# Kernel tuning notes

Hardware: AMD Instinct MI355X
Metric: run time of the kernel (lower is better)

Reference implementation:

```python
import jax, jax.numpy as jnp
import numpy as np

B, N, DM, S = 128, 1024, 64, 2
D_IN = 1 + 1 + 2 + DM  # x(1) + m(1) + u(2) + h(DM)


def setup_inputs() -> dict:
    key = jax.random.key(0)
    ks = jax.random.split(key, 12)
    return {
        "x": jax.random.normal(ks[0], (B, 1, N), jnp.float32),
        "m": jax.random.uniform(ks[1], (B, 1, N), jnp.float32),
        "u": jax.random.normal(ks[2], (B, 2, N), jnp.float32),
        "h": jax.random.normal(ks[3], (B, DM, N), jnp.float32),
        # stack of support_len row-normalized-ish adjacencies [S, N, N]
        "adj": jax.random.uniform(ks[4], (S, N, N), jnp.float32) / N,
        "W_in": jax.random.normal(ks[5], (DM, D_IN), jnp.float32) * 0.05,
        "b_in": jnp.zeros((DM,), jnp.float32),
        "W_gc": jax.random.normal(ks[6], (DM, S * DM), jnp.float32) * 0.05,
        "b_gc": jnp.zeros((DM,), jnp.float32),
        "W_out": jax.random.normal(ks[7], (DM, 2 * DM), jnp.float32) * 0.05,
        "b_out": jnp.zeros((DM,), jnp.float32),
        "W_read": jax.random.normal(ks[8], (1, 2 * DM), jnp.float32) * 0.05,
        "b_read": jnp.zeros((1,), jnp.float32),
        "prelu_w": jnp.full((1,), 0.25, jnp.float32),
    }


def _conv1x1(x, W, b):
    # Conv1d(kernel_size=1): [b,c,n] x [o,c] -> [b,o,n]
    return jnp.einsum('bcn,oc->bon', x, W) + b[None, :, None]


def reference(x, m, u, h, adj, W_in, b_in, W_gc, b_gc, W_out, b_out, W_read, b_read, prelu_w):
    # concat inputs on channel dim, then 1x1 conv to d_model
    x_in = jnp.concatenate([x, m, u, h], axis=1)            # [b, d_in, n]
    x_in = _conv1x1(x_in, W_in, b_in)                        # [b, dm, n]
    # SpatialConvOrderK (order=1, include_self=False):
    # per-support aggregation einsum('ncvl,wv->ncwl') with l==1
    agg = jnp.einsum('bcv,swv->bscw', x_in, adj)             # [b, S, dm, n]
    b_, s_, c_, n_ = agg.shape
    agg = agg.reshape(b_, s_ * c_, n_)                       # support-major concat
    gc = _conv1x1(agg, W_gc, b_gc)                           # [b, dm, n]
    out = jnp.concatenate([gc, h], axis=1)                   # [b, 2dm, n]
    out = _conv1x1(out, W_out, b_out)
    out = jnp.where(out >= 0, out, prelu_w[0] * out)         # PReLU (1 param)
    out = jnp.concatenate([out, h], axis=1)                  # [b, 2dm, n]
    return _conv1x1(out, W_read, b_read), out
```

## Files before the change

kernel.cpp:

```cpp
#include <hip/hip_runtime.h>
#include <hip/hip_bf16.h>
#include <stdint.h>

#define NB 128
#define NN 1024
#define NDM 64

typedef __bf16 bf16;
typedef __bf16 bf16x8_t __attribute__((ext_vector_type(8)));
typedef __bf16 bf16x4_t __attribute__((ext_vector_type(4)));
typedef float f32x4 __attribute__((ext_vector_type(4)));

__global__ __launch_bounds__(256) void k_prep(
    const float* __restrict__ adj,
    const float* __restrict__ W_in, const float* __restrict__ b_in,
    const float* __restrict__ W_gc, const float* __restrict__ b_gc,
    const float* __restrict__ W_out, const float* __restrict__ b_out,
    const float* __restrict__ W_read,
    bf16* __restrict__ adjb, bf16* __restrict__ WAT, float* __restrict__ WYX,
    float* __restrict__ BIAS, bf16* __restrict__ W1B, bf16* __restrict__ A2B,
    float* __restrict__ HBv) {
  const int bx = blockIdx.x;
  if (bx < 2048) {
    int i = bx * 256 + threadIdx.x;
    float4 v = reinterpret_cast<const float4*>(adj)[i];
    bf16x4_t r;
    r.x = (bf16)v.x; r.y = (bf16)v.y; r.z = (bf16)v.z; r.w = (bf16)v.w;
    reinterpret_cast<bf16x4_t*>(adjb)[i] = r;
    return;
  }
  int i = (bx - 2048) * 256 + threadIdx.x;
  if (i < 8192) {
    int r = i >> 6, cc = i & 63;
    int cq = cc >> 3, j = cc & 7;
    int c = ((cq ^ (r & 7)) << 3) + j;
    int s = r >> 6, o = r & 63;
    float val = 0.f;
    for (int k = 0; k < 64; ++k) val += W_gc[o * 128 + s * 64 + k] * W_in[k * 68 + 4 + c];
    WAT[i] = (bf16)val;
  } else if (i < 8704) {
    int idx = i - 8192;
    int r = idx >> 2, jj = idx & 3;
    int s = r >> 6, o = r & 63;
    float val = 0.f;
    for (int k = 0; k < 64; ++k) val += W_gc[o * 128 + s * 64 + k] * W_in[k * 68 + jj];
    WYX[idx] = val;
  } else if (i < 8832) {
    int r = i - 8704;
    int s = r >> 6, o = r & 63;
    float val = 0.f;
    for (int k = 0; k < 64; ++k) val += W_gc[o * 128 + s * 64 + k] * b_in[k];
    BIAS[r] = val;
  } else if (i < 12928) {
    int j = i - 8832;
    int o = j >> 6, c = j & 63;
    W1B[j] = (bf16)W_out[o * 128 + c];
  } else if (i < 18048) {
    int j = i - 12928;
    int r = j >> 6, c = j & 63;
    float val = 0.f;
    if (r < 64) val = W_out[r * 128 + 64 + c];
    else if (r == 64) val = W_read[64 + c];
    A2B[j] = (bf16)val;
  } else if (i < 18112) {
    int o = i - 18048;
    float val = b_out[o];
    for (int c = 0; c < 64; ++c) val += W_out[o * 128 + c] * b_gc[c];
    HBv[o] = val;
  }
}

__global__ __launch_bounds__(256) void k_build(
    const float* __restrict__ x, const float* __restrict__ m, const float* __restrict__ u,
    const float* __restrict__ h, const bf16* __restrict__ WAT,
    const float* __restrict__ WYX, const float* __restrict__ BIAS,
    bf16* __restrict__ Y, bf16* __restrict__ HT, float* __restrict__ out2) {
  __shared__ __align__(16) float T[64 * 128];
  __shared__ __align__(16) bf16 HTs[128 * 64];
  __shared__ __align__(16) bf16 WAs[128 * 64];
  __shared__ __align__(16) float X4L[128 * 4];
  __shared__ __align__(16) float WYXs[128 * 4];
  __shared__ __align__(16) float biasL[128];
  const int t = threadIdx.x;
  const int vb = blockIdx.x * 128;
  const int b = blockIdx.y;

  for (int i = t; i < 2048; i += 256)
    __builtin_amdgcn_global_load_lds(
        (const uint32_t*)(h + (size_t)(b * 64 + (i >> 5)) * NN + vb + (i & 31) * 4),
        (uint32_t*)&T[i * 4], 16, 0, 0);
  for (int i = t; i < 1024; i += 256)
    __builtin_amdgcn_global_load_lds((const uint32_t*)(WAT + i * 8), (uint32_t*)&WAs[i * 8], 16, 0, 0);
  if (t < 128)
    __builtin_amdgcn_global_load_lds((const uint32_t*)(WYX + t * 4), (uint32_t*)&WYXs[t * 4], 16, 0, 0);
  if (t < 32)
    __builtin_amdgcn_global_load_lds((const uint32_t*)(BIAS + t * 4), (uint32_t*)&biasL[t * 4], 16, 0, 0);
  if (t < 128) {
    float4 x4;
    x4.x = x[(size_t)b * NN + vb + t];
    x4.y = m[(size_t)b * NN + vb + t];
    x4.z = u[(size_t)(b * 2) * NN + vb + t];
    x4.w = u[(size_t)(b * 2 + 1) * NN + vb + t];
    *reinterpret_cast<float4*>(&X4L[t * 4]) = x4;
  }
  __syncthreads();

  {
    const int v = t >> 1, half = t & 1;
#pragma unroll
    for (int cc = 0; cc < 4; ++cc) {
      int cq = half * 4 + cc;
      int cbase = (cq ^ (v & 7)) << 3;
      bf16x8_t pk;
#pragma unroll
      for (int j = 0; j < 8; ++j) pk[j] = (bf16)T[(cbase + j) * 128 + v];
      *reinterpret_cast<bf16x8_t*>(&HTs[v * 64 + cq * 8]) = pk;
      *reinterpret_cast<bf16x8_t*>(&HT[((size_t)(b << 10) + vb + v) * 64 + cq * 8]) = pk;
    }
  }
  for (int i = t; i < 2048; i += 256) {
    int r = i >> 5, ck = i & 31;
    float4 hv = *reinterpret_cast<const float4*>(&T[r * 128 + ck * 4]);
    *reinterpret_cast<float4*>(&out2[(size_t)(b * 128 + 64 + r) * NN + vb + ck * 4]) = hv;
  }
  __syncthreads();

  const int wave = t >> 6, lane = t & 63;
  const int q = lane >> 4, lx = lane & 7, o16 = lane & 15;
  const int offK0 = (q ^ lx) << 3, offK1 = ((q + 4) ^ lx) << 3;

#pragma unroll
  for (int vi = 0; vi < 2; ++vi) {
    const int vt = wave + vi * 4;
    const int vrow = vt * 16 + o16;
    bf16x8_t af0 = *reinterpret_cast<const bf16x8_t*>(&HTs[vrow * 64 + offK0]);
    bf16x8_t af1 = *reinterpret_cast<const bf16x8_t*>(&HTs[vrow * 64 + offK1]);
    float4 x4r[4];
#pragma unroll
    for (int r = 0; r < 4; ++r)
      x4r[r] = *reinterpret_cast<const float4*>(&X4L[(vt * 16 + q * 4 + r) * 4]);
    const int vg = vb + vt * 16 + q * 4;
    for (int nt = 0; nt < 8; ++nt) {
      const int rr = nt * 16 + o16;
      bf16x8_t bf0 = *reinterpret_cast<const bf16x8_t*>(&WAs[rr * 64 + offK0]);
      bf16x8_t bf1 = *reinterpret_cast<const bf16x8_t*>(&WAs[rr * 64 + offK1]);
      float bsv = biasL[rr];
      float4 wy = *reinterpret_cast<const float4*>(&WYXs[rr * 4]);
      f32x4 c0;
#pragma unroll
      for (int r = 0; r < 4; ++r)
        c0[r] = bsv + wy.x * x4r[r].x + wy.y * x4r[r].y + wy.z * x4r[r].z + wy.w * x4r[r].w;
      f32x4 acc = __builtin_amdgcn_mfma_f32_16x16x32_bf16(af0, bf0, c0, 0, 0, 0);
      acc = __builtin_amdgcn_mfma_f32_16x16x32_bf16(af1, bf1, acc, 0, 0, 0);
      const int s = nt >> 2;
      const int o = rr - s * 64;
      bf16x4_t pk;
      pk.x = (bf16)acc[0]; pk.y = (bf16)acc[1]; pk.z = (bf16)acc[2]; pk.w = (bf16)acc[3];
      *reinterpret_cast<bf16x4_t*>(&Y[(size_t)(b * 64 + o) * 2048 + s * 1024 + vg]) = pk;
    }
  }
}

__global__ __launch_bounds__(512, 2) void k_gemm(
    const bf16* __restrict__ Y, const bf16* __restrict__ ADJB,
    const bf16* __restrict__ HT,
    const bf16* __restrict__ W1B, const bf16* __restrict__ A2B,
    const float* __restrict__ HBv, const float* __restrict__ W_read,
    const float* __restrict__ b_read, const float* __restrict__ prelu_w,
    float* __restrict__ out0, float* __restrict__ out2) {
  __shared__ __align__(16) union SMem {
    struct { bf16 As[3][256 * 64]; bf16 Bs[3][128 * 64]; } st;
    struct {
      bf16 gcs[4 * 128 * 72];
      bf16 W1s[64 * 72];
      bf16 A2s[80 * 72];
      float HBs[64];
      float Wrs[64];
    } ep;
  } sm;

  const int t = threadIdx.x;
  const int wave = t >> 6, lane = t & 63;
  const int lin = blockIdx.y * 32 + blockIdx.x;
  const int xcd = lin & 7, rest = lin >> 3;
  const int rowA = (xcd * 4 + (rest >> 3)) * 256;
  const int colB = (rest & 7) * 128;
  const int wm = (wave >> 1) * 64, wn = (wave & 1) * 64;
  const int fr = lane & 15;
  const int q = lane >> 4, lx = lane & 7;
  const int offK0 = (q ^ lx) << 3, offK1 = ((q + 4) ^ lx) << 3;

  f32x4 acc[4][4];
  const f32x4 zero = {0.f, 0.f, 0.f, 0.f};
#pragma unroll
  for (int i = 0; i < 4; ++i)
#pragma unroll
    for (int j = 0; j < 4; ++j) acc[i][j] = zero;

  const bf16* aSrc[4]; const bf16* bSrc[2];
#pragma unroll
  for (int j = 0; j < 4; ++j) {
    const int c = t + 512 * j;
    const int row = c >> 3;
    const int qs = ((c & 7) ^ (row & 7)) << 3;
    aSrc[j] = Y + (size_t)(rowA + row) * 2048 + qs;
  }
#pragma unroll
  for (int j = 0; j < 2; ++j) {
    const int c = t + 512 * j;
    const int row = c >> 3;
    const int qs = ((c & 7) ^ (row & 7)) << 3;
    bSrc[j] = ADJB + (size_t)(colB + row) * 1024 + qs;
  }

  auto stage = [&](int d) {
#pragma unroll
    for (int ja = 0; ja < 4; ++ja) {
      __builtin_amdgcn_global_load_lds((const uint32_t*)aSrc[ja],
                                       (uint32_t*)&sm.st.As[d][(t + 512 * ja) * 8], 16, 0, 0);
      aSrc[ja] += 64;
    }
#pragma unroll
    for (int jb = 0; jb < 2; ++jb) {
      __builtin_amdgcn_global_load_lds((const uint32_t*)bSrc[jb],
                                       (uint32_t*)&sm.st.Bs[d][(t + 512 * jb) * 8], 16, 0, 0);
      bSrc[jb] += 64;
    }
  };

  int rAb[4], rBb[4];
#pragma unroll
  for (int i = 0; i < 4; ++i) {
    rAb[i] = (wm + i * 16 + fr) * 64;
    rBb[i] = (wn + i * 16 + fr) * 64;
  }

  stage(0); stage(1); stage(2);
  asm volatile("s_waitcnt vmcnt(12)" ::: "memory");
  __builtin_amdgcn_s_barrier();
  __builtin_amdgcn_sched_barrier(0);

  bf16x8_t af0[4], bf0[4], af1[4], bf1[4];
  {
    const bf16* A_ = sm.st.As[0];
    const bf16* B_ = sm.st.Bs[0];
#pragma unroll
    for (int i = 0; i < 4; ++i) af0[i] = *reinterpret_cast<const bf16x8_t*>(&A_[rAb[i] + offK0]);
#pragma unroll
    for (int i = 0; i < 4; ++i) bf0[i] = *reinterpret_cast<const bf16x8_t*>(&B_[rBb[i] + offK0]);
  }

  int cur = 0;
  for (int kt = 0; kt < 32; ++kt) {
    const int nxt = (cur == 2) ? 0 : cur + 1;
    const bf16* A_ = sm.st.As[cur];
    const bf16* B_ = sm.st.Bs[cur];
#pragma unroll
    for (int i = 0; i < 4; ++i) af1[i] = *reinterpret_cast<const bf16x8_t*>(&A_[rAb[i] + offK1]);
#pragma unroll
    for (int i = 0; i < 4; ++i) bf1[i] = *reinterpret_cast<const bf16x8_t*>(&B_[rBb[i] + offK1]);
    asm volatile("s_waitcnt lgkmcnt(8)" ::: "memory");
    __builtin_amdgcn_sched_barrier(0);
    __builtin_amdgcn_s_setprio(1);
#pragma unroll
    for (int i = 0; i < 4; ++i)
#pragma unroll
      for (int j = 0; j < 4; ++j)
        acc[i][j] = __builtin_amdgcn_mfma_f32_16x16x32_bf16(af0[i], bf0[j], acc[i][j], 0, 0, 0);
    __builtin_amdgcn_s_setprio(0);
    asm volatile("s_waitcnt lgkmcnt(0)" ::: "memory");
    __builtin_amdgcn_sched_barrier(0);
    if (kt < 30)       asm volatile("s_waitcnt vmcnt(6)" ::: "memory");
    else if (kt == 30) asm volatile("s_waitcnt vmcnt(0)" ::: "memory");
    __builtin_amdgcn_s_barrier();
    __builtin_amdgcn_sched_barrier(0);
    if (kt < 29) {
      stage(cur);
      if (kt == 12) {
        bSrc[0] += 1024 * 1024 - 1024;
        bSrc[1] += 1024 * 1024 - 1024;
      }
    }
    if (kt < 31) {
      const bf16* An = sm.st.As[nxt];
      const bf16* Bn = sm.st.Bs[nxt];
#pragma unroll
      for (int i = 0; i < 4; ++i) af0[i] = *reinterpret_cast<const bf16x8_t*>(&An[rAb[i] + offK0]);
#pragma unroll
      for (int i = 0; i < 4; ++i) bf0[i] = *reinterpret_cast<const bf16x8_t*>(&Bn[rBb[i] + offK0]);
    }
    __builtin_amdgcn_s_setprio(1);
#pragma unroll
    for (int i = 0; i < 4; ++i)
#pragma unroll
      for (int j = 0; j < 4; ++j)
        acc[i][j] = __builtin_amdgcn_mfma_f32_16x16x32_bf16(af1[i], bf1[j], acc[i][j], 0, 0, 0);
    __builtin_amdgcn_s_setprio(0);
    cur = nxt;
  }

  {
    const int r = t >> 3, c8 = t & 7;
    *reinterpret_cast<bf16x8_t*>(&sm.ep.W1s[r * 72 + c8 * 8]) =
        *reinterpret_cast<const bf16x8_t*>(&W1B[t * 8]);
  }
  for (int i = t; i < 640; i += 512) {
    const int r = i >> 3, c8 = i & 7;
    *reinterpret_cast<bf16x8_t*>(&sm.ep.A2s[r * 72 + c8 * 8]) =
        *reinterpret_cast<const bf16x8_t*>(&A2B[i * 8]);
  }
  if (t < 64) { sm.ep.HBs[t] = HBv[t]; sm.ep.Wrs[t] = W_read[t]; }
  const float pw = prelu_w[0];
  const float br = b_read[0];

  {
    const int b2w = wm >> 6;
#pragma unroll
    for (int i = 0; i < 4; ++i) {
      const int cc0 = i * 16 + q * 4;
#pragma unroll
      for (int j = 0; j < 4; ++j) {
        const int wl = wn + j * 16 + fr;
        bf16x4_t r;
        r.x = (bf16)acc[i][j][0]; r.y = (bf16)acc[i][j][1];
        r.z = (bf16)acc[i][j][2]; r.w = (bf16)acc[i][j][3];
        *reinterpret_cast<bf16x4_t*>(&sm.ep.gcs[b2w * 9216 + wl * 72 + cc0]) = r;
      }
    }
  }
  __syncthreads();

  const int b2 = wave >> 1, jh = wave & 1;
  const int b = (rowA >> 6) + b2;

  f32x4 acc2[5][4];
#pragma unroll
  for (int i = 0; i < 5; ++i)
#pragma unroll
    for (int j = 0; j < 4; ++j) {
      if (i < 4) {
        f32x4 c0;
#pragma unroll
        for (int r = 0; r < 4; ++r) c0[r] = sm.ep.HBs[i * 16 + q * 4 + r];
        acc2[i][j] = c0;
      } else {
        acc2[i][j] = zero;
      }
    }

#pragma unroll
  for (int k2 = 0; k2 < 64; k2 += 32) {
    bf16x8_t af2[4], bf2[4];
#pragma unroll
    for (int i = 0; i < 4; ++i)
      af2[i] = *reinterpret_cast<const bf16x8_t*>(&sm.ep.W1s[(i * 16 + fr) * 72 + k2 + q * 8]);
#pragma unroll
    for (int j = 0; j < 4; ++j)
      bf2[j] = *reinterpret_cast<const bf16x8_t*>(&sm.ep.gcs[b2 * 9216 + (jh * 64 + j * 16 + fr) * 72 + k2 + q * 8]);
#pragma unroll
    for (int i = 0; i < 4; ++i)
#pragma unroll
      for (int j = 0; j < 4; ++j)
        acc2[i][j] = __builtin_amdgcn_mfma_f32_16x16x32_bf16(af2[i], bf2[j], acc2[i][j], 0, 0, 0);
  }

#pragma unroll
  for (int k2 = 0; k2 < 64; k2 += 32) {
    const int off = k2 ? offK1 : offK0;
    bf16x8_t bh[4], af3[5];
#pragma unroll
    for (int j = 0; j < 4; ++j) {
      const int w = colB + jh * 64 + j * 16 + fr;
      bh[j] = *reinterpret_cast<const bf16x8_t*>(&HT[((size_t)(b << 10) + w) * 64 + off]);
    }
#pragma unroll
    for (int i = 0; i < 5; ++i)
      af3[i] = *reinterpret_cast<const bf16x8_t*>(&sm.ep.A2s[(i * 16 + fr) * 72 + k2 + q * 8]);
#pragma unroll
    for (int i = 0; i < 5; ++i)
#pragma unroll
      for (int j = 0; j < 4; ++j)
        acc2[i][j] = __builtin_amdgcn_mfma_f32_16x16x32_bf16(af3[i], bh[j], acc2[i][j], 0, 0, 0);
  }

  float rd[4] = {0.f, 0.f, 0.f, 0.f};
#pragma unroll
  for (int i = 0; i < 4; ++i) {
#pragma unroll
    for (int r = 0; r < 4; ++r) {
      const int o = i * 16 + q * 4 + r;
      const float wr = sm.ep.Wrs[o];
#pragma unroll
      for (int j = 0; j < 4; ++j) {
        const int wg = colB + jh * 64 + j * 16 + fr;
        float val = acc2[i][j][r];
        val = val >= 0.f ? val : pw * val;
        out2[(size_t)(b * 128 + o) * 1024 + wg] = val;
        rd[j] += wr * val;
      }
    }
  }
#pragma unroll
  for (int j = 0; j < 4; ++j) {
    rd[j] += __shfl_xor(rd[j], 16, 64);
    rd[j] += __shfl_xor(rd[j], 32, 64);
  }
  if (lane < 16) {
#pragma unroll
    for (int j = 0; j < 4; ++j) {
      const int wg = colB + jh * 64 + j * 16 + lane;
      out0[(size_t)b * 1024 + wg] = rd[j] + acc2[4][j][0] + br;
    }
  }
}

extern "C" void kernel_launch(void* const* d_in, const int* in_sizes, int n_in,
                              void* d_out, int out_size, void* d_ws, size_t ws_size,
                              hipStream_t stream) {
  (void)in_sizes; (void)n_in; (void)out_size; (void)ws_size;
  const float* x       = (const float*)d_in[0];
  const float* m       = (const float*)d_in[1];
  const float* u       = (const float*)d_in[2];
  const float* h       = (const float*)d_in[3];
  const float* adj     = (const float*)d_in[4];
  const float* W_in    = (const float*)d_in[5];
  const float* b_in    = (const float*)d_in[6];
  const float* W_gc    = (const float*)d_in[7];
  const float* b_gc    = (const float*)d_in[8];
  const float* W_out   = (const float*)d_in[9];
  const float* b_out   = (const float*)d_in[10];
  const float* W_read  = (const float*)d_in[11];
  const float* b_read  = (const float*)d_in[12];
  const float* prelu_w = (const float*)d_in[13];

  char* ws = (char*)d_ws;
  bf16*  Y    = (bf16*)(ws);
  bf16*  ADJB = (bf16*)(ws + 33554432);
  bf16*  HT   = (bf16*)(ws + 37748736);
  bf16*  WAT  = (bf16*)(ws + 54525952);
  float* WYX  = (float*)(ws + 54542336);
  float* BIAS = (float*)(ws + 54544384);
  bf16*  W1B  = (bf16*)(ws + 54544896);
  bf16*  A2B  = (bf16*)(ws + 54553088);
  float* HBv  = (float*)(ws + 54563328);

  float* out0 = (float*)d_out;
  float* out2 = out0 + 131072;

  hipLaunchKernelGGL(k_prep,  dim3(2119),     dim3(256), 0, stream,
                     adj, W_in, b_in, W_gc, b_gc, W_out, b_out, W_read,
                     ADJB, WAT, WYX, BIAS, W1B, A2B, HBv);
  hipLaunchKernelGGL(k_build, dim3(8, 128),   dim3(256), 0, stream,
                     x, m, u, h, WAT, WYX, BIAS, Y, HT, out2);
  hipLaunchKernelGGL(k_gemm,  dim3(32, 8),    dim3(512), 0, stream,
                     Y, ADJB, HT, W1B, A2B, HBv, W_read, b_read, prelu_w, out0, out2);
}
```

Baseline: 178.1 us.

## Move adj bf16 conversion into build kernel and coalesce Y/HT stores via LDS

The adjacency fp32→bf16 conversion moves out of k_prep into 256 extra blocks of k_build, so it overlaps with the build work and k_prep shrinks to a tiny launch. In k_build, the MFMA outputs are staged in a swizzled LDS buffer that reuses the T array, then written to Y as 16-byte contiguous rows instead of scattered 8-byte stores. HT is also written from LDS in fully contiguous 16-byte chunks. The cost is an extra __syncthreads and LDS round trip, and the k_build grid now carries heterogeneous blocks.

```diff
diff --git a/kernel.cpp b/kernel.cpp
--- a/kernel.cpp
+++ b/kernel.cpp
@@ -12,24 +12,14 @@
 typedef float f32x4 __attribute__((ext_vector_type(4)));
 
 __global__ __launch_bounds__(256) void k_prep(
-    const float* __restrict__ adj,
     const float* __restrict__ W_in, const float* __restrict__ b_in,
     const float* __restrict__ W_gc, const float* __restrict__ b_gc,
     const float* __restrict__ W_out, const float* __restrict__ b_out,
     const float* __restrict__ W_read,
-    bf16* __restrict__ adjb, bf16* __restrict__ WAT, float* __restrict__ WYX,
+    bf16* __restrict__ WAT, float* __restrict__ WYX,
     float* __restrict__ BIAS, bf16* __restrict__ W1B, bf16* __restrict__ A2B,
     float* __restrict__ HBv) {
-  const int bx = blockIdx.x;
-  if (bx < 2048) {
-    int i = bx * 256 + threadIdx.x;
-    float4 v = reinterpret_cast<const float4*>(adj)[i];
-    bf16x4_t r;
-    r.x = (bf16)v.x; r.y = (bf16)v.y; r.z = (bf16)v.z; r.w = (bf16)v.w;
-    reinterpret_cast<bf16x4_t*>(adjb)[i] = r;
-    return;
-  }
-  int i = (bx - 2048) * 256 + threadIdx.x;
+  int i = blockIdx.x * 256 + threadIdx.x;
   if (i < 8192) {
     int r = i >> 6, cc = i & 63;
     int cq = cc >> 3, j = cc & 7;
@@ -72,9 +62,11 @@
 
 __global__ __launch_bounds__(256) void k_build(
     const float* __restrict__ x, const float* __restrict__ m, const float* __restrict__ u,
-    const float* __restrict__ h, const bf16* __restrict__ WAT,
+    const float* __restrict__ h, const float* __restrict__ adj,
+    const bf16* __restrict__ WAT,
     const float* __restrict__ WYX, const float* __restrict__ BIAS,
-    bf16* __restrict__ Y, bf16* __restrict__ HT, float* __restrict__ out2) {
+    bf16* __restrict__ adjb, bf16* __restrict__ Y, bf16* __restrict__ HT,
+    float* __restrict__ out2) {
   __shared__ __align__(16) float T[64 * 128];
   __shared__ __align__(16) bf16 HTs[128 * 64];
   __shared__ __align__(16) bf16 WAs[128 * 64];
@@ -82,6 +74,20 @@
   __shared__ __align__(16) float WYXs[128 * 4];
   __shared__ __align__(16) float biasL[128];
   const int t = threadIdx.x;
+
+  if (blockIdx.x >= 8) {
+    const int chunk = (blockIdx.x - 8) * 128 + blockIdx.y;
+#pragma unroll
+    for (int k2 = 0; k2 < 8; ++k2) {
+      int i = chunk * 2048 + k2 * 256 + t;
+      float4 v = reinterpret_cast<const float4*>(adj)[i];
+      bf16x4_t r;
+      r.x = (bf16)v.x; r.y = (bf16)v.y; r.z = (bf16)v.z; r.w = (bf16)v.w;
+      reinterpret_cast<bf16x4_t*>(adjb)[i] = r;
+    }
+    return;
+  }
+
   const int vb = blockIdx.x * 128;
   const int b = blockIdx.y;
 
@@ -115,7 +121,6 @@
 #pragma unroll
       for (int j = 0; j < 8; ++j) pk[j] = (bf16)T[(cbase + j) * 128 + v];
       *reinterpret_cast<bf16x8_t*>(&HTs[v * 64 + cq * 8]) = pk;
-      *reinterpret_cast<bf16x8_t*>(&HT[((size_t)(b << 10) + vb + v) * 64 + cq * 8]) = pk;
     }
   }
   for (int i = t; i < 2048; i += 256) {
@@ -125,9 +130,20 @@
   }
   __syncthreads();
 
+  {
+    const bf16* HTs_b = HTs;
+#pragma unroll
+    for (int p = 0; p < 4; ++p) {
+      int i = p * 256 + t;
+      bf16x8_t v = *reinterpret_cast<const bf16x8_t*>(&HTs_b[i * 8]);
+      *reinterpret_cast<bf16x8_t*>(&HT[((size_t)(b << 10) + vb) * 64 + i * 8]) = v;
+    }
+  }
+
   const int wave = t >> 6, lane = t & 63;
   const int q = lane >> 4, lx = lane & 7, o16 = lane & 15;
   const int offK0 = (q ^ lx) << 3, offK1 = ((q + 4) ^ lx) << 3;
+  bf16* YT = reinterpret_cast<bf16*>(T);
 
 #pragma unroll
   for (int vi = 0; vi < 2; ++vi) {
@@ -139,7 +155,6 @@
 #pragma unroll
     for (int r = 0; r < 4; ++r)
       x4r[r] = *reinterpret_cast<const float4*>(&X4L[(vt * 16 + q * 4 + r) * 4]);
-    const int vg = vb + vt * 16 + q * 4;
     for (int nt = 0; nt < 8; ++nt) {
       const int rr = nt * 16 + o16;
       bf16x8_t bf0 = *reinterpret_cast<const bf16x8_t*>(&WAs[rr * 64 + offK0]);
@@ -152,12 +167,23 @@
         c0[r] = bsv + wy.x * x4r[r].x + wy.y * x4r[r].y + wy.z * x4r[r].z + wy.w * x4r[r].w;
       f32x4 acc = __builtin_amdgcn_mfma_f32_16x16x32_bf16(af0, bf0, c0, 0, 0, 0);
       acc = __builtin_amdgcn_mfma_f32_16x16x32_bf16(af1, bf1, acc, 0, 0, 0);
-      const int s = nt >> 2;
-      const int o = rr - s * 64;
       bf16x4_t pk;
       pk.x = (bf16)acc[0]; pk.y = (bf16)acc[1]; pk.z = (bf16)acc[2]; pk.w = (bf16)acc[3];
-      *reinterpret_cast<bf16x4_t*>(&Y[(size_t)(b * 64 + o) * 2048 + s * 1024 + vg]) = pk;
-    }
+      const int c8 = (vt * 4 + q) ^ ((rr & 7) << 2);
+      *reinterpret_cast<bf16x4_t*>(&YT[rr * 128 + c8 * 4]) = pk;
+    }
+  }
+  __syncthreads();
+
+#pragma unroll
+  for (int p = 0; p < 8; ++p) {
+    int i = p * 256 + t;
+    int ro = i >> 4;
+    int cc = (i & 15) * 2;
+    int cs = cc ^ ((ro & 7) << 2);
+    bf16x8_t v = *reinterpret_cast<const bf16x8_t*>(&YT[ro * 128 + cs * 4]);
+    int s = ro >> 6, o = ro & 63;
+    *reinterpret_cast<bf16x8_t*>(&Y[(size_t)(b * 64 + o) * 2048 + s * 1024 + vb + (i & 15) * 8]) = v;
   }
 }
 
@@ -447,11 +473,11 @@
   float* out0 = (float*)d_out;
   float* out2 = out0 + 131072;
 
-  hipLaunchKernelGGL(k_prep,  dim3(2119),     dim3(256), 0, stream,
-                     adj, W_in, b_in, W_gc, b_gc, W_out, b_out, W_read,
-                     ADJB, WAT, WYX, BIAS, W1B, A2B, HBv);
-  hipLaunchKernelGGL(k_build, dim3(8, 128),   dim3(256), 0, stream,
-                     x, m, u, h, WAT, WYX, BIAS, Y, HT, out2);
+  hipLaunchKernelGGL(k_prep,  dim3(71),       dim3(256), 0, stream,
+                     W_in, b_in, W_gc, b_gc, W_out, b_out, W_read,
+                     WAT, WYX, BIAS, W1B, A2B, HBv);
+  hipLaunchKernelGGL(k_build, dim3(10, 128),  dim3(256), 0, stream,
+                     x, m, u, h, adj, WAT, WYX, BIAS, ADJB, Y, HT, out2);
   hipLaunchKernelGGL(k_gemm,  dim3(32, 8),    dim3(512), 0, stream,
                      Y, ADJB, HT, W1B, A2B, HBv, W_read, b_read, prelu_w, out0, out2);
 }
```

Measured after the change: 175.0 us (median of 2 runs). About the same (-1.7%).
